# Kernel optimization log

Measured on AMD Instinct MI355X. Metric: run time of the kernel, lower is better.

Reference implementation:

```python
import jax, jax.numpy as jnp
import numpy as np

B, T, D, H, L, W = 32, 512, 256, 8, 2, 10
NQ = 10000
HD = D // H


def setup_inputs():
    key = jax.random.key(0)
    ks = jax.random.split(key, 16)
    def n(k, shape, s=0.02):
        return jax.random.normal(k, shape, jnp.float32) * s
    return {
        "q": jax.random.randint(ks[0], (B, T), 0, NQ),
        "s": jax.random.randint(ks[1], (B, T), 0, 2),
        "q_embed": n(ks[2], (NQ + 1, D)),
        "s_embed": n(ks[3], (2, D)),
        "pos_embed": n(ks[4], (512, D)),
        "fusion_w": n(ks[5], (2 * D, D)),
        "fusion_b": jnp.zeros((D,), jnp.float32),
        "in_proj_w": n(ks[6], (L, D, 3 * D)),
        "in_proj_b": jnp.zeros((L, 3 * D), jnp.float32),
        "out_proj_w": n(ks[7], (L, D, D)),
        "out_proj_b": jnp.zeros((L, D), jnp.float32),
        "ln1_g": jnp.ones((L, D), jnp.float32),
        "ln1_b": jnp.zeros((L, D), jnp.float32),
        "ln2_g": jnp.ones((L, D), jnp.float32),
        "ln2_b": jnp.zeros((L, D), jnp.float32),
        "ff1_w": n(ks[8], (L, D, 4 * D)),
        "ff1_b": jnp.zeros((L, 4 * D), jnp.float32),
        "ff2_w": n(ks[9], (L, 4 * D, D)),
        "ff2_b": jnp.zeros((L, D), jnp.float32),
        "sw1": n(ks[10], (6, 32), 0.1),
        "sb1": jnp.zeros((32,), jnp.float32),
        "sw2": n(ks[11], (32, D // 4), 0.1),
        "sb2": jnp.zeros((D // 4,), jnp.float32),
        "cw1": n(ks[12], (D + D // 4, D)),
        "cb1": jnp.zeros((D,), jnp.float32),
        "cw2": n(ks[13], (D, 1)),
        "cb2": jnp.zeros((1,), jnp.float32),
    }


def _ln(x, g, b):
    mu = jnp.mean(x, -1, keepdims=True)
    var = jnp.mean(jnp.square(x - mu), -1, keepdims=True)
    return (x - mu) * jax.lax.rsqrt(var + 1e-5) * g + b


def _sliding_sum(x, w):
    # sum over trailing window of size w ending at each t, via prefix sums
    c = jnp.concatenate([jnp.zeros((x.shape[0], 1), x.dtype), jnp.cumsum(x, axis=1)], axis=1)
    t = jnp.arange(x.shape[1])
    return c[:, t + 1] - c[:, jnp.maximum(t + 1 - w, 0)]


def _stats(s, mask):
    # vectorized version of _extract_statistics (prefix-sum sliding windows)
    mf = mask.astype(jnp.float32)
    sf = s.astype(jnp.float32) * mf
    valid = _sliding_sum(mf, W)
    correct_rate = _sliding_sum(sf, W) / (valid + 1e-6)
    rc = _sliding_sum(mf, 5)
    recent_correct = _sliding_sum(sf, 5) / (rc + 1e-6)
    trans = ((s[:, 1:] != s[:, :-1]) & mask[:, 1:] & mask[:, :-1]).astype(jnp.float32)
    diff = jnp.concatenate([jnp.zeros((s.shape[0], 1), jnp.float32), trans], axis=1)
    change_rate = _sliding_sum(diff, W - 1) / (valid + 1e-6)
    # max consecutive equal run within each trailing window of size W
    sp = jnp.pad(s, ((0, 0), (W - 1, 0)))
    mp = jnp.pad(mask, ((0, 0), (W - 1, 0)))
    win_s = [sp[:, j:j + T] for j in range(W)]
    win_m = [mp[:, j:j + T] for j in range(W)]
    run = win_m[0].astype(jnp.float32)
    mx = run
    for j in range(1, W):  # fixed small window, not a data-dim loop
        eq = (win_s[j] == win_s[j - 1]) & win_m[j - 1]
        run = win_m[j].astype(jnp.float32) * (jnp.where(eq, run, 0.0) + 1.0)
        mx = jnp.maximum(mx, run)
    rel = jnp.broadcast_to(jnp.arange(T, dtype=jnp.float32) / max(T, 100), s.shape)
    cov = valid / W
    return jnp.stack([correct_rate, recent_correct, change_rate, mx / W, rel, cov], axis=-1)


def reference(q, s, q_embed, s_embed, pos_embed, fusion_w, fusion_b, in_proj_w, in_proj_b,
              out_proj_w, out_proj_b, ln1_g, ln1_b, ln2_g, ln2_b, ff1_w, ff1_b, ff2_w, ff2_b,
              sw1, sb1, sw2, sb2, cw1, cb1, cw2, cb2):
    mask = s >= 0
    qm = jnp.where(mask, q, 0)
    sm = jnp.where(mask, s, 0)
    h = jnp.concatenate([q_embed[qm], s_embed[sm]], axis=-1)  # [B,T,2D]
    h = jax.nn.relu(h @ fusion_w + fusion_b) + pos_embed[:T][None]
    causal = jnp.tril(jnp.ones((T, T), bool))
    allowed = causal[None, None] & mask[:, None, None, :]
    scale = 1.0 / (HD ** 0.5)
    for l in range(L):
        qkv = h @ in_proj_w[l] + in_proj_b[l]
        qh, kh, vh = jnp.split(qkv, 3, axis=-1)
        qh = qh.reshape(B, T, H, HD).transpose(0, 2, 1, 3)
        kh = kh.reshape(B, T, H, HD).transpose(0, 2, 1, 3)
        vh = vh.reshape(B, T, H, HD).transpose(0, 2, 1, 3)
        scores = jnp.einsum('bhqd,bhkd->bhqk', qh, kh) * scale
        scores = jnp.where(allowed, scores, -1e9)
        attn = jax.nn.softmax(scores, axis=-1)
        o = jnp.einsum('bhqk,bhkd->bhqd', attn, vh).transpose(0, 2, 1, 3).reshape(B, T, D)
        h = _ln(h + (o @ out_proj_w[l] + out_proj_b[l]), ln1_g[l], ln1_b[l])
        ff = jax.nn.gelu(h @ ff1_w[l] + ff1_b[l], approximate=False) @ ff2_w[l] + ff2_b[l]
        h = _ln(h + ff, ln2_g[l], ln2_b[l])
    sfeat = _stats(sm, mask)  # [B,T,6]
    semb = jax.nn.relu(sfeat @ sw1 + sb1) @ sw2 + sb2  # [B,T,D//4]
    comb = jnp.concatenate([h, semb], axis=-1)
    logits = (jax.nn.relu(comb @ cw1 + cb1) @ cw2 + cb2)[..., 0]
    return jnp.where(mask, logits, -1e9)
```

## Files before the change

kernel.cpp:

```cpp
#include <hip/hip_runtime.h>
#include <hip/hip_bf16.h>
#include <cmath>


using short8 = __attribute__((ext_vector_type(8))) short;
using short4v = __attribute__((ext_vector_type(4))) short;
using f32x4  = __attribute__((ext_vector_type(4))) float;

__device__ inline float gelu_f(float x) {
    return 0.5f * x * (1.0f + erff(x * 0.70710678118654752f));
}

__device__ inline short f2bf(float x) {
    union { float f; unsigned u; } v; v.f = x;
    return (short)((v.u + 0x7fffu + ((v.u >> 16) & 1u)) >> 16);
}

__device__ inline float bf2f(short v) {
    union { unsigned u; float f; } x; x.u = ((unsigned)(unsigned short)v) << 16;
    return x.f;
}

__device__ inline unsigned packbf(float lo, float hi) {
    union { float f; unsigned u; } a, b; a.f = lo; b.f = hi;
    unsigned ra = (a.u + 0x7fffu + ((a.u >> 16) & 1u)) >> 16;
    unsigned rb = (b.u + 0x7fffu + ((b.u >> 16) & 1u)) >> 16;
    return (rb << 16) | (ra & 0xffffu);
}

#define GLOAD16(gp, lp) __builtin_amdgcn_global_load_lds( \
    (const __attribute__((address_space(1))) void*)(gp), \
    (__attribute__((address_space(3))) void*)(lp), 16, 0, 0)

__global__ __launch_bounds__(256) void prep(
    const float* __restrict__ fusion_w, const float* __restrict__ in_proj_w,
    const float* __restrict__ out_proj_w, const float* __restrict__ ff1_w,
    const float* __restrict__ ff2_w, const float* __restrict__ cw1,
    short* __restrict__ wts,
    const int* __restrict__ s,
    short* __restrict__ semb,
    const float* __restrict__ sw1, const float* __restrict__ sb1,
    const float* __restrict__ sw2, const float* __restrict__ sb2)
{
    __shared__ float tile[32][33];
    __shared__ float sv_sh[512];
    __shared__ float m_sh[512];
    __shared__ float sw2_sh[2048];

    if (blockIdx.x < 1744) {
        const int b0[10]      = {0,128,320,512,576,640,896,1152,1408,1664};
        const int Ks[10]      = {512,256,256,256,256,256,256,1024,1024,320};
        const int Ns[10]      = {256,768,768,256,256,1024,1024,256,256,256};
        const int sidx[10]    = {0,1,1,2,2,3,3,4,4,5};
        const size_t soff[10] = {0,0,196608,0,65536,0,262144,0,262144,0};
        const size_t doff[10] = {0,131072,327680,524288,589824,655360,917504,1179648,1441792,1703936};
        const float* srcs[6] = {fusion_w, in_proj_w, out_proj_w, ff1_w, ff2_w, cw1};
        int bid = blockIdx.x;
        int mi = 0;
        while (mi < 9 && bid >= b0[mi + 1]) ++mi;
        int bl = bid - b0[mi];
        int K = Ks[mi], N = Ns[mi];
        int tx = bl % (N >> 5), ty = bl / (N >> 5);
        const float* src = srcs[sidx[mi]] + soff[mi];
        short* dst = wts + doff[mi];
        int c = threadIdx.x & 31, r = threadIdx.x >> 5;
#pragma unroll
        for (int i = 0; i < 4; ++i)
            tile[r + i * 8][c] = src[(size_t)(ty * 32 + r + i * 8) * N + tx * 32 + c];
        __syncthreads();
#pragma unroll
        for (int i = 0; i < 4; ++i)
            dst[(size_t)(tx * 32 + r + i * 8) * K + ty * 32 + c] = f2bf(tile[c][r + i * 8]);
    } else {
        const int b = blockIdx.x - 1744;
        const int tt = threadIdx.x;
        for (int t = tt; t < 512; t += 256) {
            int sval = s[b * 512 + t];
            bool mk = sval >= 0;
            sv_sh[t] = mk ? (float)sval : 0.f;
            m_sh[t] = mk ? 1.f : 0.f;
        }
        for (int i = tt; i < 2048; i += 256) sw2_sh[i] = sw2[i];
        __syncthreads();
        for (int half = 0; half < 2; ++half) {
            const int t = tt + half * 256;
            float mf10 = 0, sf10 = 0, mf5 = 0, sf5 = 0, d9 = 0;
#pragma unroll
            for (int k = 0; k < 10; ++k) {
                int idx = t - k;
                if (idx >= 0) {
                    float mv = m_sh[idx], sv = sv_sh[idx];
                    mf10 += mv; sf10 += sv;
                    if (k < 5) { mf5 += mv; sf5 += sv; }
                    if (k < 9 && idx >= 1) {
                        if (sv != sv_sh[idx - 1] && mv > 0.5f && m_sh[idx - 1] > 0.5f) d9 += 1.f;
                    }
                }
            }
            float run, mx;
            {
                int x0 = t - 9;
                run = (x0 >= 0) ? m_sh[x0] : 0.f;
                mx = run;
#pragma unroll
                for (int j = 1; j < 10; ++j) {
                    int xc = t + j - 9, xp = xc - 1;
                    float sc = (xc >= 0) ? sv_sh[xc] : 0.f;
                    float sp = (xp >= 0) ? sv_sh[xp] : 0.f;
                    float mc = (xc >= 0) ? m_sh[xc] : 0.f;
                    float mp = (xp >= 0) ? m_sh[xp] : 0.f;
                    bool eq = (sc == sp) && (mp > 0.5f);
                    run = (mc > 0.5f) ? ((eq ? run : 0.f) + 1.f) : 0.f;
                    mx = fmaxf(mx, run);
                }
            }
            float f[6];
            f[0] = sf10 / (mf10 + 1e-6f);
            f[1] = sf5 / (mf5 + 1e-6f);
            f[2] = d9 / (mf10 + 1e-6f);
            f[3] = mx * 0.1f;
            f[4] = (float)t * (1.f / 512.f);
            f[5] = mf10 * 0.1f;

            float hid[32];
#pragma unroll
            for (int j2 = 0; j2 < 32; ++j2) {
                float a = sb1[j2];
#pragma unroll
                for (int i = 0; i < 6; ++i) a = fmaf(f[i], sw1[i * 32 + j2], a);
                hid[j2] = fmaxf(a, 0.f);
            }
            short* orow = semb + ((size_t)b * 512 + t) * 64;
            for (int c = 0; c < 64; c += 4) {
                float v0 = sb2[c], v1 = sb2[c + 1], v2 = sb2[c + 2], v3 = sb2[c + 3];
#pragma unroll
                for (int j2 = 0; j2 < 32; ++j2) {
                    float hh = hid[j2];
                    v0 = fmaf(hh, sw2_sh[j2 * 64 + c], v0);
                    v1 = fmaf(hh, sw2_sh[j2 * 64 + c + 1], v1);
                    v2 = fmaf(hh, sw2_sh[j2 * 64 + c + 2], v2);
                    v3 = fmaf(hh, sw2_sh[j2 * 64 + c + 3], v3);
                }
                short4v o; o[0] = f2bf(v0); o[1] = f2bf(v1); o[2] = f2bf(v2); o[3] = f2bf(v3);
                *(short4v*)(orow + c) = o;
            }
        }
    }
}

template<int EPI, int KTOT, int MS>
__global__ __launch_bounds__(512) void kbs(
    const short* __restrict__ A, const short* __restrict__ Wt,
    const float* __restrict__ bias,
    short* __restrict__ o0, short* __restrict__ o1, short* __restrict__ o2,
    const float* __restrict__ pos,
    const int* __restrict__ qi, const int* __restrict__ si,
    const float* __restrict__ qe, const float* __restrict__ se)
{
    constexpr int BN = 64;
    constexpr int SPR = KTOT / 8;
    constexpr int NK = KTOT / 32;
    __shared__ short Bs[BN * KTOT];
    const int tid = threadIdx.x, lane = tid & 63, wv = tid >> 6;
    const int lg = lane >> 4, lr = lane & 15;
    const int n0 = blockIdx.y * BN;

#pragma unroll
    for (int i = 0; i < (BN * SPR) / 512; ++i) {
        int slot = i * 512 + tid;
        int n = slot / SPR, posn = slot % SPR;
        int g = posn ^ (n & 7);
        GLOAD16(Wt + (size_t)(n0 + n) * KTOT + g * 8, &Bs[slot * 8]);
    }
    __syncthreads();

#pragma unroll
    for (int m = 0; m < MS; ++m) {
        const int row0 = (blockIdx.x * MS + m) * 128 + wv * 16;
        short8 af[NK];
        if constexpr (EPI == 0) {
            int row = row0 + lr;
            int sv = si[row];
            bool mk = sv >= 0;
            const float* b0 = qe + (size_t)(mk ? qi[row] : 0) * 256;
            const float* b1 = se + (size_t)(mk ? sv : 0) * 256;
#pragma unroll
            for (int kk = 0; kk < NK; ++kk) {
                const float* p = ((kk < 8) ? b0 + kk * 32 : b1 + (kk - 8) * 32) + lg * 8;
                float4 v0 = *(const float4*)p;
                float4 v1 = *(const float4*)(p + 4);
                short8 o;
                o[0] = f2bf(v0.x); o[1] = f2bf(v0.y); o[2] = f2bf(v0.z); o[3] = f2bf(v0.w);
                o[4] = f2bf(v1.x); o[5] = f2bf(v1.y); o[6] = f2bf(v1.z); o[7] = f2bf(v1.w);
                af[kk] = o;
            }
        } else {
            const short* ar = A + (size_t)(row0 + lr) * KTOT + lg * 8;
#pragma unroll
            for (int kk = 0; kk < NK; ++kk)
                af[kk] = *(const short8*)(ar + kk * 32);
        }

        f32x4 acc[4] = {};
#pragma unroll
        for (int kk = 0; kk < NK; ++kk) {
#pragma unroll
            for (int j = 0; j < 4; ++j) {
                int n = j * 16 + lr;
                short8 b = *(const short8*)&Bs[n * KTOT + (((kk * 4 + lg) ^ (n & 7)) << 3)];
                acc[j] = __builtin_amdgcn_mfma_f32_16x16x32_bf16(af[kk], b, acc[j], 0, 0, 0);
            }
        }

        if constexpr (EPI == 0) {
#pragma unroll
            for (int j = 0; j < 4; ++j)
#pragma unroll
            for (int r = 0; r < 4; ++r) {
                int row = row0 + lg * 4 + r;
                int col = n0 + j * 16 + lr;
                float x = acc[j][r] + bias[col];
                x = fmaxf(x, 0.f) + pos[(size_t)(row & 511) * 256 + col];
                o0[(size_t)row * 256 + col] = f2bf(x);
            }
        } else if constexpr (EPI == 1) {
#pragma unroll
            for (int j = 0; j < 4; ++j)
#pragma unroll
            for (int r = 0; r < 4; ++r) {
                int row = row0 + lg * 4 + r;
                int gcol = n0 + j * 16 + lr;
                int t = row & 511, bg = row >> 9;
                int sec = gcol >> 8, cc = gcol & 255;
                int h = cc >> 5, d = cc & 31, bh = bg * 8 + h;
                short v = f2bf(acc[j][r] + bias[gcol]);
                if (sec == 0)      o0[((size_t)bh * 512 + t) * 32 + d] = v;
                else if (sec == 1) o1[((size_t)bh * 512 + t) * 32 + d] = v;
                else {
                    int kl = t & 31;
                    o2[(size_t)bh * 16384 + (size_t)(t >> 5) * 1024 +
                       (size_t)((kl >> 2) & 3) * 256 + d * 8 + (((kl & 3) << 1) | ((kl >> 4) & 1))] = v;
                }
            }
        } else {
#pragma unroll
            for (int j = 0; j < 4; ++j)
#pragma unroll
            for (int r = 0; r < 4; ++r) {
                int row = row0 + lg * 4 + r;
                int gcol = n0 + j * 16 + lr;
                float x = acc[j][r] + bias[gcol];
                o0[(size_t)row * 1024 + gcol] = f2bf(gelu_f(x));
            }
        }
    }
}

template<int EPI, int KTOT>
__global__ __launch_bounds__(512) void kfull(
    const short* __restrict__ A, const short* __restrict__ A2,
    const short* __restrict__ Wt, const float* __restrict__ bias,
    short* __restrict__ hb,
    const float* __restrict__ gamma, const float* __restrict__ beta,
    const float* __restrict__ cw2v, const float* __restrict__ cb2,
    const int* __restrict__ smask, float* __restrict__ outlog)
{
    constexpr int NCH = (KTOT + 127) / 128;
    constexpr int KA = (EPI == 1) ? 256 : KTOT;
    __shared__ short Bs[256 * 128];
    __shared__ float redS[32][4];
    __shared__ float redQ[32][4];
    const int tid = threadIdx.x, lane = tid & 63, wv = tid >> 6;
    const int lg = lane >> 4, lr = lane & 15;
    const int wr = wv >> 2, wc = wv & 3;
    const int row0 = blockIdx.x * 32 + wr * 16;

    f32x4 acc[4] = {};
    short8 af[4];

#pragma unroll
    for (int c = 0; c < NCH; ++c) {
        const int ck = (KTOT - c * 128 >= 128) ? 128 : (KTOT - c * 128);
        const int spr = ck >> 3;
        if (c) __syncthreads();
        for (int i = 0; i < (256 * ck) / 8; i += 512) {
            int slot = i + tid;
            int n = slot / spr, posn = slot % spr;
            int g = posn ^ (n & 7);
            GLOAD16(Wt + (size_t)n * KTOT + c * 128 + g * 8, &Bs[slot * 8]);
        }
        const int nkk = ck >> 5;
        if (EPI == 1 && c == 2) {
            const short* ar2 = A2 + (size_t)(row0 + lr) * 64 + lg * 8;
            af[0] = *(const short8*)(ar2);
            af[1] = *(const short8*)(ar2 + 32);
        } else {
            const short* ar = A + (size_t)(row0 + lr) * KA + c * 128 + lg * 8;
#pragma unroll
            for (int kk = 0; kk < 4; ++kk)
                if (kk < nkk) af[kk] = *(const short8*)(ar + kk * 32);
        }
        __syncthreads();
#pragma unroll
        for (int kk = 0; kk < 4; ++kk) {
            if (kk >= nkk) break;
#pragma unroll
            for (int j = 0; j < 4; ++j) {
                int n = wc * 64 + j * 16 + lr;
                short8 b = *(const short8*)&Bs[n * ck + (((kk * 4 + lg) ^ (n & 7)) << 3)];
                acc[j] = __builtin_amdgcn_mfma_f32_16x16x32_bf16(af[kk], b, acc[j], 0, 0, 0);
            }
        }
    }

    if constexpr (EPI == 0) {
        float ps[4] = {0.f, 0.f, 0.f, 0.f}, pq[4] = {0.f, 0.f, 0.f, 0.f};
#pragma unroll
        for (int j = 0; j < 4; ++j)
#pragma unroll
        for (int r = 0; r < 4; ++r) {
            int row = row0 + lg * 4 + r;
            int col = wc * 64 + j * 16 + lr;
            float x = acc[j][r] + bias[col] + bf2f(hb[(size_t)row * 256 + col]);
            acc[j][r] = x;
            ps[r] += x; pq[r] += x * x;
        }
#pragma unroll
        for (int off = 1; off < 16; off <<= 1)
#pragma unroll
            for (int r = 0; r < 4; ++r) {
                ps[r] += __shfl_xor(ps[r], off);
                pq[r] += __shfl_xor(pq[r], off);
            }
        if (lr == 0) {
#pragma unroll
            for (int r = 0; r < 4; ++r) {
                int rl = wr * 16 + lg * 4 + r;
                redS[rl][wc] = ps[r]; redQ[rl][wc] = pq[r];
            }
        }
        __syncthreads();
#pragma unroll
        for (int r = 0; r < 4; ++r) {
            int rl = wr * 16 + lg * 4 + r;
            int row = row0 + lg * 4 + r;
            float sm = redS[rl][0] + redS[rl][1] + redS[rl][2] + redS[rl][3];
            float sq = redQ[rl][0] + redQ[rl][1] + redQ[rl][2] + redQ[rl][3];
            float mu = sm * (1.f / 256.f);
            float var = sq * (1.f / 256.f) - mu * mu;
            float rstd = rsqrtf(var + 1e-5f);
#pragma unroll
            for (int j = 0; j < 4; ++j) {
                int col = wc * 64 + j * 16 + lr;
                float y = (acc[j][r] - mu) * rstd * gamma[col] + beta[col];
                hb[(size_t)row * 256 + col] = f2bf(y);
            }
        }
    } else {
        float p[4] = {0.f, 0.f, 0.f, 0.f};
#pragma unroll
        for (int j = 0; j < 4; ++j)
#pragma unroll
        for (int r = 0; r < 4; ++r) {
            int col = wc * 64 + j * 16 + lr;
            float v = fmaxf(acc[j][r] + bias[col], 0.f);
            p[r] += v * cw2v[col];
        }
#pragma unroll
        for (int off = 1; off < 16; off <<= 1)
#pragma unroll
            for (int r = 0; r < 4; ++r) p[r] += __shfl_xor(p[r], off);
        if (lr == 0) {
#pragma unroll
            for (int r = 0; r < 4; ++r)
                redS[wr * 16 + lg * 4 + r][wc] = p[r];
        }
        __syncthreads();
        if (tid < 32) {
            int row = blockIdx.x * 32 + tid;
            float v = redS[tid][0] + redS[tid][1] + redS[tid][2] + redS[tid][3] + cb2[0];
            outlog[row] = (smask[row] >= 0) ? v : -1e9f;
        }
    }
}

__global__ __launch_bounds__(256) void attn_mfma(
    const short* __restrict__ Qg, const short* __restrict__ Kg,
    const short* __restrict__ VTg, short* __restrict__ O)
{
    __shared__ unsigned Wp[4][2][2][16][20];
    const int bh = blockIdx.x >> 2, part = blockIdx.x & 3;
    const int b = bh >> 3, h = bh & 7;
    const int wv = threadIdx.x >> 6, lane = threadIdx.x & 63;
    const int lg = lane >> 4, lr = lane & 15;
    const int slot = part * 4 + wv;
    const short* Qbh = Qg + (size_t)bh * 16384;
    const short* Kbh = Kg + (size_t)bh * 16384;
    const short* Vbh = VTg + (size_t)bh * 16384;
    const float cs = 0.25503590f;

    const int tA = slot, tB = 31 - slot;
    const int qA0 = tA << 4, qB0 = tB << 4;
    const int nA = tA >> 1, nB = tB >> 1;
    short8 qaA = *(const short8*)(Qbh + (size_t)(qA0 + lr) * 32 + lg * 8);
    short8 qaB = *(const short8*)(Qbh + (size_t)(qB0 + lr) * 32 + lg * 8);
    f32x4 oA0 = {}, oA1 = {}, oB0 = {}, oB1 = {};
    float lA[4] = {0.f, 0.f, 0.f, 0.f};
    float lB[4] = {0.f, 0.f, 0.f, 0.f};

    auto chunk = [&](int c, int q0, int nfull, const short8& qa,
                     const short8& kf0, const short8& kf1,
                     const short8& vf0, const short8& vf1,
                     f32x4& o0, f32x4& o1, float* l_, int slab) {
        int kc = c << 5;
        int par = c & 1;
        f32x4 s0 = {}, s1 = {};
        s0 = __builtin_amdgcn_mfma_f32_16x16x32_bf16(qa, kf0, s0, 0, 0, 0);
        s1 = __builtin_amdgcn_mfma_f32_16x16x32_bf16(qa, kf1, s1, 0, 0, 0);
        float p0[4], p1[4];
        if (c < nfull) {
#pragma unroll
            for (int r = 0; r < 4; ++r) {
                p0[r] = exp2f(s0[r] * cs);
                p1[r] = exp2f(s1[r] * cs);
            }
        } else {
#pragma unroll
            for (int r = 0; r < 4; ++r) {
                int qq = q0 + lg * 4 + r;
                p0[r] = (kc + lr)      > qq ? 0.f : exp2f(s0[r] * cs);
                p1[r] = (kc + 16 + lr) > qq ? 0.f : exp2f(s1[r] * cs);
            }
        }
#pragma unroll
        for (int r = 0; r < 4; ++r) {
            l_[r] += p0[r] + p1[r];
            Wp[wv][slab][par][lg * 4 + r][lr] = packbf(p0[r], p1[r]);
        }
        short8 pa = *(const short8*)&Wp[wv][slab][par][lr][lg * 4];
        o0 = __builtin_amdgcn_mfma_f32_16x16x32_bf16(pa, vf0, o0, 0, 0, 0);
        o1 = __builtin_amdgcn_mfma_f32_16x16x32_bf16(pa, vf1, o1, 0, 0, 0);
    };

    int c = 0;
    for (; c <= nA; ++c) {
        int kc = c << 5;
        short8 kf0 = *(const short8*)(Kbh + (size_t)(kc + lr) * 32 + lg * 8);
        short8 kf1 = *(const short8*)(Kbh + (size_t)(kc + 16 + lr) * 32 + lg * 8);
        short8 vf0 = *(const short8*)(Vbh + (size_t)c * 1024 + lg * 256 + lr * 8);
        short8 vf1 = *(const short8*)(Vbh + (size_t)c * 1024 + lg * 256 + (lr + 16) * 8);
        chunk(c, qB0, nB, qaB, kf0, kf1, vf0, vf1, oB0, oB1, lB, 1);
        chunk(c, qA0, nA, qaA, kf0, kf1, vf0, vf1, oA0, oA1, lA, 0);
    }
    for (; c <= nB; ++c) {
        int kc = c << 5;
        short8 kf0 = *(const short8*)(Kbh + (size_t)(kc + lr) * 32 + lg * 8);
        short8 kf1 = *(const short8*)(Kbh + (size_t)(kc + 16 + lr) * 32 + lg * 8);
        short8 vf0 = *(const short8*)(Vbh + (size_t)c * 1024 + lg * 256 + lr * 8);
        short8 vf1 = *(const short8*)(Vbh + (size_t)c * 1024 + lg * 256 + (lr + 16) * 8);
        chunk(c, qB0, nB, qaB, kf0, kf1, vf0, vf1, oB0, oB1, lB, 1);
    }

#pragma unroll
    for (int off = 1; off < 16; off <<= 1)
#pragma unroll
        for (int r = 0; r < 4; ++r) {
            lA[r] += __shfl_xor(lA[r], off);
            lB[r] += __shfl_xor(lB[r], off);
        }
#pragma unroll
    for (int r = 0; r < 4; ++r) {
        float invA = 1.f / lA[r];
        size_t roA = ((size_t)b * 512 + qA0 + lg * 4 + r) * 256 + h * 32;
        O[roA + lr] = f2bf(oA0[r] * invA);
        O[roA + 16 + lr] = f2bf(oA1[r] * invA);
        float invB = 1.f / lB[r];
        size_t roB = ((size_t)b * 512 + qB0 + lg * 4 + r) * 256 + h * 32;
        O[roB + lr] = f2bf(oB0[r] * invB);
        O[roB + 16 + lr] = f2bf(oB1[r] * invB);
    }
}

extern "C" void kernel_launch(void* const* d_in, const int* in_sizes, int n_in,
                              void* d_out, int out_size, void* d_ws, size_t ws_size,
                              hipStream_t stream) {
    const int*   q         = (const int*)d_in[0];
    const int*   s         = (const int*)d_in[1];
    const float* q_embed   = (const float*)d_in[2];
    const float* s_embed   = (const float*)d_in[3];
    const float* pos_embed = (const float*)d_in[4];
    const float* fusion_w  = (const float*)d_in[5];
    const float* fusion_b  = (const float*)d_in[6];
    const float* in_proj_w = (const float*)d_in[7];
    const float* in_proj_b = (const float*)d_in[8];
    const float* out_proj_w= (const float*)d_in[9];
    const float* out_proj_b= (const float*)d_in[10];
    const float* ln1_g     = (const float*)d_in[11];
    const float* ln1_b     = (const float*)d_in[12];
    const float* ln2_g     = (const float*)d_in[13];
    const float* ln2_b     = (const float*)d_in[14];
    const float* ff1_w     = (const float*)d_in[15];
    const float* ff1_b     = (const float*)d_in[16];
    const float* ff2_w     = (const float*)d_in[17];
    const float* ff2_b     = (const float*)d_in[18];
    const float* sw1       = (const float*)d_in[19];
    const float* sb1       = (const float*)d_in[20];
    const float* sw2       = (const float*)d_in[21];
    const float* sb2       = (const float*)d_in[22];
    const float* cw1       = (const float*)d_in[23];
    const float* cb1       = (const float*)d_in[24];
    const float* cw2       = (const float*)d_in[25];
    const float* cb2       = (const float*)d_in[26];
    float* out = (float*)d_out;

    char* base = (char*)d_ws;
    short* hb   = (short*)(base);
    short* bufA = (short*)(base + 8388608);
    short* att  = (short*)(base + 41943040);
    short* Qg   = (short*)(base + 50331648);
    short* Kg   = (short*)(base + 58720256);
    short* VTg  = (short*)(base + 67108864);
    short* semb = (short*)(base + 75497472);
    short* wts  = (short*)(base + 77594624);

    const size_t W_FUSION = 0, W_INPROJ0 = 131072, W_INPROJ1 = 327680;
    const size_t W_OUTPROJ0 = 524288, W_OUTPROJ1 = 589824;
    const size_t W_FF1_0 = 655360, W_FF1_1 = 917504;
    const size_t W_FF2_0 = 1179648, W_FF2_1 = 1441792;
    const size_t W_CW1 = 1703936;

    prep<<<1776, 256, 0, stream>>>(fusion_w, in_proj_w, out_proj_w,
                                   ff1_w, ff2_w, cw1, wts,
                                   s, semb, sw1, sb1, sw2, sb2);
    kbs<0, 512, 1><<<dim3(128, 4), 512, 0, stream>>>(nullptr,
        wts + W_FUSION, fusion_b, hb, nullptr, nullptr,
        pos_embed, q, s, q_embed, s_embed);
    for (int l = 0; l < 2; ++l) {
        kbs<1, 256, 2><<<dim3(64, 12), 512, 0, stream>>>(hb,
            wts + (l ? W_INPROJ1 : W_INPROJ0), in_proj_b + l * 768,
            Qg, Kg, VTg, nullptr, nullptr, nullptr, nullptr, nullptr);
        attn_mfma<<<1024, 256, 0, stream>>>(Qg, Kg, VTg, att);
        kfull<0, 256><<<512, 512, 0, stream>>>(att, nullptr,
            wts + (l ? W_OUTPROJ1 : W_OUTPROJ0), out_proj_b + l * 256,
            hb, ln1_g + l * 256, ln1_b + l * 256,
            nullptr, nullptr, nullptr, nullptr);
        kbs<2, 256, 2><<<dim3(64, 16), 512, 0, stream>>>(hb,
            wts + (l ? W_FF1_1 : W_FF1_0), ff1_b + l * 1024,
            bufA, nullptr, nullptr, nullptr, nullptr, nullptr, nullptr, nullptr);
        kfull<0, 1024><<<512, 512, 0, stream>>>(bufA, nullptr,
            wts + (l ? W_FF2_1 : W_FF2_0), ff2_b + l * 256,
            hb, ln2_g + l * 256, ln2_b + l * 256,
            nullptr, nullptr, nullptr, nullptr);
    }
    kfull<1, 320><<<512, 512, 0, stream>>>(hb, semb,
        wts + W_CW1, cb1, nullptr, nullptr, nullptr,
        cw2, cb2, s, out);
}
```

Measured before the change: 290.3 us.

## Give each wave two 16-row M-tiles sharing B fragments in GEMM kernels

Each wave now computes two 16-row tiles at once, so every B fragment read from LDS feeds two MFMAs instead of one. This applies to both the kbs GEMMs and the fused LayerNorm/classifier kernels, and the grids shrink accordingly. In kbs the A-fragment global loads are now issued before the barrier, so they overlap with the weight staging into LDS. The cost is more accumulator and fragment registers per wave and fewer blocks, which lowers parallelism and risks occupancy loss or register spills, especially in the 1024-K kfull.

After: 306.9 us. +5.7%, slower.

```diff
diff --git a/kernel.cpp b/kernel.cpp
--- a/kernel.cpp
+++ b/kernel.cpp
@@ -148,7 +148,7 @@
     }
 }
 
-template<int EPI, int KTOT, int MS>
+template<int EPI, int KTOT>
 __global__ __launch_bounds__(512) void kbs(
     const short* __restrict__ A, const short* __restrict__ Wt,
     const float* __restrict__ bias,
@@ -164,6 +164,7 @@
     const int tid = threadIdx.x, lane = tid & 63, wv = tid >> 6;
     const int lg = lane >> 4, lr = lane & 15;
     const int n0 = blockIdx.y * BN;
+    const int row0 = blockIdx.x * 256 + wv * 32;
 
 #pragma unroll
     for (int i = 0; i < (BN * SPR) / 512; ++i) {
@@ -172,14 +173,12 @@
         int g = posn ^ (n & 7);
         GLOAD16(Wt + (size_t)(n0 + n) * KTOT + g * 8, &Bs[slot * 8]);
     }
-    __syncthreads();
-
-#pragma unroll
-    for (int m = 0; m < MS; ++m) {
-        const int row0 = (blockIdx.x * MS + m) * 128 + wv * 16;
-        short8 af[NK];
+
+    short8 af[2][NK];
+#pragma unroll
+    for (int gg = 0; gg < 2; ++gg) {
         if constexpr (EPI == 0) {
-            int row = row0 + lr;
+            int row = row0 + gg * 16 + lr;
             int sv = si[row];
             bool mk = sv >= 0;
             const float* b0 = qe + (size_t)(mk ? qi[row] : 0) * 256;
@@ -192,34 +191,39 @@
                 short8 o;
                 o[0] = f2bf(v0.x); o[1] = f2bf(v0.y); o[2] = f2bf(v0.z); o[3] = f2bf(v0.w);
                 o[4] = f2bf(v1.x); o[5] = f2bf(v1.y); o[6] = f2bf(v1.z); o[7] = f2bf(v1.w);
-                af[kk] = o;
+                af[gg][kk] = o;
             }
         } else {
-            const short* ar = A + (size_t)(row0 + lr) * KTOT + lg * 8;
+            const short* ar = A + (size_t)(row0 + gg * 16 + lr) * KTOT + lg * 8;
 #pragma unroll
             for (int kk = 0; kk < NK; ++kk)
-                af[kk] = *(const short8*)(ar + kk * 32);
-        }
-
-        f32x4 acc[4] = {};
-#pragma unroll
-        for (int kk = 0; kk < NK; ++kk) {
-#pragma unroll
-            for (int j = 0; j < 4; ++j) {
-                int n = j * 16 + lr;
-                short8 b = *(const short8*)&Bs[n * KTOT + (((kk * 4 + lg) ^ (n & 7)) << 3)];
-                acc[j] = __builtin_amdgcn_mfma_f32_16x16x32_bf16(af[kk], b, acc[j], 0, 0, 0);
-            }
-        }
-
+                af[gg][kk] = *(const short8*)(ar + kk * 32);
+        }
+    }
+    __syncthreads();
+
+    f32x4 acc[2][4] = {};
+#pragma unroll
+    for (int kk = 0; kk < NK; ++kk) {
+#pragma unroll
+        for (int j = 0; j < 4; ++j) {
+            int n = j * 16 + lr;
+            short8 b = *(const short8*)&Bs[n * KTOT + (((kk * 4 + lg) ^ (n & 7)) << 3)];
+            acc[0][j] = __builtin_amdgcn_mfma_f32_16x16x32_bf16(af[0][kk], b, acc[0][j], 0, 0, 0);
+            acc[1][j] = __builtin_amdgcn_mfma_f32_16x16x32_bf16(af[1][kk], b, acc[1][j], 0, 0, 0);
+        }
+    }
+
+#pragma unroll
+    for (int gg = 0; gg < 2; ++gg) {
         if constexpr (EPI == 0) {
 #pragma unroll
             for (int j = 0; j < 4; ++j)
 #pragma unroll
             for (int r = 0; r < 4; ++r) {
-                int row = row0 + lg * 4 + r;
+                int row = row0 + gg * 16 + lg * 4 + r;
                 int col = n0 + j * 16 + lr;
-                float x = acc[j][r] + bias[col];
+                float x = acc[gg][j][r] + bias[col];
                 x = fmaxf(x, 0.f) + pos[(size_t)(row & 511) * 256 + col];
                 o0[(size_t)row * 256 + col] = f2bf(x);
             }
@@ -228,12 +232,12 @@
             for (int j = 0; j < 4; ++j)
 #pragma unroll
             for (int r = 0; r < 4; ++r) {
-                int row = row0 + lg * 4 + r;
+                int row = row0 + gg * 16 + lg * 4 + r;
                 int gcol = n0 + j * 16 + lr;
                 int t = row & 511, bg = row >> 9;
                 int sec = gcol >> 8, cc = gcol & 255;
                 int h = cc >> 5, d = cc & 31, bh = bg * 8 + h;
-                short v = f2bf(acc[j][r] + bias[gcol]);
+                short v = f2bf(acc[gg][j][r] + bias[gcol]);
                 if (sec == 0)      o0[((size_t)bh * 512 + t) * 32 + d] = v;
                 else if (sec == 1) o1[((size_t)bh * 512 + t) * 32 + d] = v;
                 else {
@@ -247,9 +251,9 @@
             for (int j = 0; j < 4; ++j)
 #pragma unroll
             for (int r = 0; r < 4; ++r) {
-                int row = row0 + lg * 4 + r;
+                int row = row0 + gg * 16 + lg * 4 + r;
                 int gcol = n0 + j * 16 + lr;
-                float x = acc[j][r] + bias[gcol];
+                float x = acc[gg][j][r] + bias[gcol];
                 o0[(size_t)row * 1024 + gcol] = f2bf(gelu_f(x));
             }
         }
@@ -268,15 +272,15 @@
     constexpr int NCH = (KTOT + 127) / 128;
     constexpr int KA = (EPI == 1) ? 256 : KTOT;
     __shared__ short Bs[256 * 128];
-    __shared__ float redS[32][4];
-    __shared__ float redQ[32][4];
+    __shared__ float redS[64][4];
+    __shared__ float redQ[64][4];
     const int tid = threadIdx.x, lane = tid & 63, wv = tid >> 6;
     const int lg = lane >> 4, lr = lane & 15;
     const int wr = wv >> 2, wc = wv & 3;
-    const int row0 = blockIdx.x * 32 + wr * 16;
-
-    f32x4 acc[4] = {};
-    short8 af[4];
+    const int row0 = blockIdx.x * 64 + wr * 32;
+
+    f32x4 acc[2][4] = {};
+    short8 af[2][4];
 
 #pragma unroll
     for (int c = 0; c < NCH; ++c) {
@@ -291,14 +295,20 @@
         }
         const int nkk = ck >> 5;
         if (EPI == 1 && c == 2) {
-            const short* ar2 = A2 + (size_t)(row0 + lr) * 64 + lg * 8;
-            af[0] = *(const short8*)(ar2);
-            af[1] = *(const short8*)(ar2 + 32);
+#pragma unroll
+            for (int gg = 0; gg < 2; ++gg) {
+                const short* ar2 = A2 + (size_t)(row0 + gg * 16 + lr) * 64 + lg * 8;
+                af[gg][0] = *(const short8*)(ar2);
+                af[gg][1] = *(const short8*)(ar2 + 32);
+            }
         } else {
-            const short* ar = A + (size_t)(row0 + lr) * KA + c * 128 + lg * 8;
-#pragma unroll
-            for (int kk = 0; kk < 4; ++kk)
-                if (kk < nkk) af[kk] = *(const short8*)(ar + kk * 32);
+#pragma unroll
+            for (int gg = 0; gg < 2; ++gg) {
+                const short* ar = A + (size_t)(row0 + gg * 16 + lr) * KA + c * 128 + lg * 8;
+#pragma unroll
+                for (int kk = 0; kk < 4; ++kk)
+                    if (kk < nkk) af[gg][kk] = *(const short8*)(ar + kk * 32);
+            }
         }
         __syncthreads();
 #pragma unroll
@@ -308,42 +318,51 @@
             for (int j = 0; j < 4; ++j) {
                 int n = wc * 64 + j * 16 + lr;
                 short8 b = *(const short8*)&Bs[n * ck + (((kk * 4 + lg) ^ (n & 7)) << 3)];
-                acc[j] = __builtin_amdgcn_mfma_f32_16x16x32_bf16(af[kk], b, acc[j], 0, 0, 0);
+                acc[0][j] = __builtin_amdgcn_mfma_f32_16x16x32_bf16(af[0][kk], b, acc[0][j], 0, 0, 0);
+                acc[1][j] = __builtin_amdgcn_mfma_f32_16x16x32_bf16(af[1][kk], b, acc[1][j], 0, 0, 0);
             }
         }
     }
 
     if constexpr (EPI == 0) {
-        float ps[4] = {0.f, 0.f, 0.f, 0.f}, pq[4] = {0.f, 0.f, 0.f, 0.f};
+        float ps[2][4] = {}, pq[2][4] = {};
+#pragma unroll
+        for (int gg = 0; gg < 2; ++gg)
 #pragma unroll
         for (int j = 0; j < 4; ++j)
 #pragma unroll
         for (int r = 0; r < 4; ++r) {
-            int row = row0 + lg * 4 + r;
+            int row = row0 + gg * 16 + lg * 4 + r;
             int col = wc * 64 + j * 16 + lr;
-            float x = acc[j][r] + bias[col] + bf2f(hb[(size_t)row * 256 + col]);
-            acc[j][r] = x;
-            ps[r] += x; pq[r] += x * x;
+            float x = acc[gg][j][r] + bias[col] + bf2f(hb[(size_t)row * 256 + col]);
+            acc[gg][j][r] = x;
+            ps[gg][r] += x; pq[gg][r] += x * x;
         }
 #pragma unroll
         for (int off = 1; off < 16; off <<= 1)
 #pragma unroll
-            for (int r = 0; r < 4; ++r) {
-                ps[r] += __shfl_xor(ps[r], off);
-                pq[r] += __shfl_xor(pq[r], off);
+            for (int gg = 0; gg < 2; ++gg)
+#pragma unroll
+            for (int r = 0; r < 4; ++r) {
+                ps[gg][r] += __shfl_xor(ps[gg][r], off);
+                pq[gg][r] += __shfl_xor(pq[gg][r], off);
             }
         if (lr == 0) {
 #pragma unroll
-            for (int r = 0; r < 4; ++r) {
-                int rl = wr * 16 + lg * 4 + r;
-                redS[rl][wc] = ps[r]; redQ[rl][wc] = pq[r];
+            for (int gg = 0; gg < 2; ++gg)
+#pragma unroll
+            for (int r = 0; r < 4; ++r) {
+                int rl = wr * 32 + gg * 16 + lg * 4 + r;
+                redS[rl][wc] = ps[gg][r]; redQ[rl][wc] = pq[gg][r];
             }
         }
         __syncthreads();
 #pragma unroll
+        for (int gg = 0; gg < 2; ++gg)
+#pragma unroll
         for (int r = 0; r < 4; ++r) {
-            int rl = wr * 16 + lg * 4 + r;
-            int row = row0 + lg * 4 + r;
+            int rl = wr * 32 + gg * 16 + lg * 4 + r;
+            int row = blockIdx.x * 64 + rl;
             float sm = redS[rl][0] + redS[rl][1] + redS[rl][2] + redS[rl][3];
             float sq = redQ[rl][0] + redQ[rl][1] + redQ[rl][2] + redQ[rl][3];
             float mu = sm * (1.f / 256.f);
@@ -352,32 +371,38 @@
 #pragma unroll
             for (int j = 0; j < 4; ++j) {
                 int col = wc * 64 + j * 16 + lr;
-                float y = (acc[j][r] - mu) * rstd * gamma[col] + beta[col];
+                float y = (acc[gg][j][r] - mu) * rstd * gamma[col] + beta[col];
                 hb[(size_t)row * 256 + col] = f2bf(y);
             }
         }
     } else {
-        float p[4] = {0.f, 0.f, 0.f, 0.f};
+        float p[2][4] = {};
+#pragma unroll
+        for (int gg = 0; gg < 2; ++gg)
 #pragma unroll
         for (int j = 0; j < 4; ++j)
 #pragma unroll
         for (int r = 0; r < 4; ++r) {
             int col = wc * 64 + j * 16 + lr;
-            float v = fmaxf(acc[j][r] + bias[col], 0.f);
-            p[r] += v * cw2v[col];
+            float v = fmaxf(acc[gg][j][r] + bias[col], 0.f);
+            p[gg][r] += v * cw2v[col];
         }
 #pragma unroll
         for (int off = 1; off < 16; off <<= 1)
 #pragma unroll
-            for (int r = 0; r < 4; ++r) p[r] += __shfl_xor(p[r], off);
+            for (int gg = 0; gg < 2; ++gg)
+#pragma unroll
+            for (int r = 0; r < 4; ++r) p[gg][r] += __shfl_xor(p[gg][r], off);
         if (lr == 0) {
 #pragma unroll
+            for (int gg = 0; gg < 2; ++gg)
+#pragma unroll
             for (int r = 0; r < 4; ++r)
-                redS[wr * 16 + lg * 4 + r][wc] = p[r];
+                redS[wr * 32 + gg * 16 + lg * 4 + r][wc] = p[gg][r];
         }
         __syncthreads();
-        if (tid < 32) {
-            int row = blockIdx.x * 32 + tid;
+        if (tid < 64) {
+            int row = blockIdx.x * 64 + tid;
             float v = redS[tid][0] + redS[tid][1] + redS[tid][2] + redS[tid][3] + cb2[0];
             outlog[row] = (smask[row] >= 0) ? v : -1e9f;
         }
@@ -532,27 +557,27 @@
     prep<<<1776, 256, 0, stream>>>(fusion_w, in_proj_w, out_proj_w,
                                    ff1_w, ff2_w, cw1, wts,
                                    s, semb, sw1, sb1, sw2, sb2);
-    kbs<0, 512, 1><<<dim3(128, 4), 512, 0, stream>>>(nullptr,
+    kbs<0, 512><<<dim3(64, 4), 512, 0, stream>>>(nullptr,
         wts + W_FUSION, fusion_b, hb, nullptr, nullptr,
         pos_embed, q, s, q_embed, s_embed);
     for (int l = 0; l < 2; ++l) {
-        kbs<1, 256, 2><<<dim3(64, 12), 512, 0, stream>>>(hb,
+        kbs<1, 256><<<dim3(64, 12), 512, 0, stream>>>(hb,
             wts + (l ? W_INPROJ1 : W_INPROJ0), in_proj_b + l * 768,
             Qg, Kg, VTg, nullptr, nullptr, nullptr, nullptr, nullptr);
         attn_mfma<<<1024, 256, 0, stream>>>(Qg, Kg, VTg, att);
-        kfull<0, 256><<<512, 512, 0, stream>>>(att, nullptr,
+        kfull<0, 256><<<256, 512, 0, stream>>>(att, nullptr,
             wts + (l ? W_OUTPROJ1 : W_OUTPROJ0), out_proj_b + l * 256,
             hb, ln1_g + l * 256, ln1_b + l * 256,
             nullptr, nullptr, nullptr, nullptr);
-        kbs<2, 256, 2><<<dim3(64, 16), 512, 0, stream>>>(hb,
+        kbs<2, 256><<<dim3(64, 16), 512, 0, stream>>>(hb,
             wts + (l ? W_FF1_1 : W_FF1_0), ff1_b + l * 1024,
             bufA, nullptr, nullptr, nullptr, nullptr, nullptr, nullptr, nullptr);
-        kfull<0, 1024><<<512, 512, 0, stream>>>(bufA, nullptr,
+        kfull<0, 1024><<<256, 512, 0, stream>>>(bufA, nullptr,
             wts + (l ? W_FF2_1 : W_FF2_0), ff2_b + l * 256,
             hb, ln2_g + l * 256, ln2_b + l * 256,
             nullptr, nullptr, nullptr, nullptr);
     }
-    kfull<1, 320><<<512, 512, 0, stream>>>(hb, semb,
+    kfull<1, 320><<<256, 512, 0, stream>>>(hb, semb,
         wts + W_CW1, cb1, nullptr, nullptr, nullptr,
         cw2, cb2, s, out);
 }
```
